# Optimization experiments

Hardware: AMD Instinct MI355X
Metric: run time of the kernel (lower is better)

The kernel has to match this reference:

```python
import jax, jax.numpy as jnp
import numpy as np

B, LQ, D, NH, NL, NP, DFFN = 16, 900, 256, 8, 4, 4, 2048
HD = D // NH
SHAPES = [(128, 128), (64, 64), (32, 32), (16, 16)]
LIN = sum(h * w for h, w in SHAPES)


def setup_inputs():
    ks = jax.random.split(jax.random.key(0), 24)
    p = lambda k, s: jax.random.normal(k, s, jnp.float32) * 0.02
    z = lambda s: jnp.zeros(s, jnp.float32)
    return {
        "queries": jax.random.normal(ks[0], (B, LQ, D), jnp.float32),
        "features": jax.random.normal(ks[1], (B, LIN, D), jnp.float32),
        "reference_points": jax.random.uniform(ks[2], (B, LQ, NL, 2), jnp.float32),
        "q_pos": jax.random.normal(ks[3], (B, LQ, D), jnp.float32),
        "in_proj_w": p(ks[4], (3 * D, D)), "in_proj_b": z((3 * D,)),
        "out_proj_w": p(ks[5], (D, D)), "out_proj_b": z((D,)),
        "value_proj_w": p(ks[6], (D, D)), "value_proj_b": z((D,)),
        "samp_w": p(ks[7], (NH * NL * NP * 2, D)),
        "samp_b": jax.random.uniform(ks[8], (NH * NL * NP * 2,), jnp.float32, -0.5, 0.5),
        "attw_w": p(ks[9], (NH * NL * NP, D)), "attw_b": z((NH * NL * NP,)),
        "msout_w": p(ks[10], (D, D)), "msout_b": z((D,)),
        "ffn_w1": p(ks[11], (DFFN, D)), "ffn_b1": z((DFFN,)),
        "ffn_w2": p(ks[12], (D, DFFN)), "ffn_b2": z((D,)),
        "ln1_g": jnp.ones((D,), jnp.float32), "ln1_b": z((D,)),
        "ln2_g": jnp.ones((D,), jnp.float32), "ln2_b": z((D,)),
        "ln3_g": jnp.ones((D,), jnp.float32), "ln3_b": z((D,)),
        "kv_spatial_shapes": np.array(SHAPES, np.int32),
        "level_start_index": np.concatenate([[0], np.cumsum([h * w for h, w in SHAPES])[:-1]]).astype(np.int32),
    }


def _ln(x, g, b, eps=1e-5):
    m = x.mean(-1, keepdims=True)
    v = ((x - m) ** 2).mean(-1, keepdims=True)
    return (x - m) * jax.lax.rsqrt(v + eps) * g + b


def _mha(q, k, v, wqkv, bqkv, wo, bo):
    wq, wk, wv = wqkv[:D], wqkv[D:2 * D], wqkv[2 * D:]
    bq, bk, bv = bqkv[:D], bqkv[D:2 * D], bqkv[2 * D:]
    qh = (q @ wq.T + bq).reshape(B, LQ, NH, HD)
    kh = (k @ wk.T + bk).reshape(B, LQ, NH, HD)
    vh = (v @ wv.T + bv).reshape(B, LQ, NH, HD)
    s = jnp.einsum("bqhd,bkhd->bhqk", qh, kh) / jnp.sqrt(jnp.float32(HD))
    a = jax.nn.softmax(s, axis=-1)
    o = jnp.einsum("bhqk,bkhd->bqhd", a, vh).reshape(B, LQ, D)
    return o @ wo.T + bo


def _ms_deform(value, loc, attw):
    # value (B,LIN,NH,HD); loc (B,LQ,NH,NL,NP,2) normalized; attw (B,LQ,NH,NL,NP)
    out = jnp.zeros((B, LQ, NH, HD), jnp.float32)
    start = 0
    for l, (hl, wl) in enumerate(SHAPES):
        v = value[:, start:start + hl * wl].transpose(0, 2, 1, 3)  # (B,NH,hl*wl,HD)
        g = loc[:, :, :, l]  # (B,LQ,NH,NP,2)
        # grid_sample align_corners=False pixel coords
        x = g[..., 0] * wl - 0.5
        y = g[..., 1] * hl - 0.5
        x0 = jnp.floor(x); y0 = jnp.floor(y)
        fx = x - x0; fy = y - y0
        x0 = x0.astype(jnp.int32); y0 = y0.astype(jnp.int32)
        acc = jnp.zeros((B, LQ, NH, NP, HD), jnp.float32)
        for dy, wy in ((0, 1.0 - fy), (1, fy)):
            for dx, wx in ((0, 1.0 - fx), (1, fx)):
                xi = x0 + dx; yi = y0 + dy
                valid = (xi >= 0) & (xi < wl) & (yi >= 0) & (yi < hl)
                idx = jnp.clip(yi, 0, hl - 1) * wl + jnp.clip(xi, 0, wl - 1)
                idx = idx.transpose(0, 2, 1, 3).reshape(B, NH, LQ * NP)
                s = jnp.take_along_axis(v, idx[..., None], axis=2)
                s = s.reshape(B, NH, LQ, NP, HD).transpose(0, 2, 1, 3, 4)
                w = jnp.where(valid, wy * wx, 0.0)  # zero-padding outside
                acc = acc + s * w[..., None]
        out = out + (acc * attw[:, :, :, l, :, None]).sum(3)
        start += hl * wl
    return out.reshape(B, LQ, D)


def reference(queries, features, reference_points, q_pos, in_proj_w, in_proj_b, out_proj_w, out_proj_b, value_proj_w, value_proj_b, samp_w, samp_b, attw_w, attw_b, msout_w, msout_b, ffn_w1, ffn_b1, ffn_w2, ffn_b2, ln1_g, ln1_b, ln2_g, ln2_b, ln3_g, ln3_b, kv_spatial_shapes, level_start_index):
    qk = queries + q_pos
    x = _ln(queries + _mha(qk, qk, queries, in_proj_w, in_proj_b, out_proj_w, out_proj_b), ln1_g, ln1_b)
    # deformable multi-scale cross attention
    q2 = x + q_pos
    value = (features @ value_proj_w.T + value_proj_b).reshape(B, LIN, NH, HD)
    off = (q2 @ samp_w.T + samp_b).reshape(B, LQ, NH, NL, NP, 2)
    attw = jax.nn.softmax((q2 @ attw_w.T + attw_b).reshape(B, LQ, NH, NL * NP), axis=-1).reshape(B, LQ, NH, NL, NP)
    norm = jnp.stack([jnp.asarray(kv_spatial_shapes)[:, 1], jnp.asarray(kv_spatial_shapes)[:, 0]], -1).astype(jnp.float32)  # (NL,2)=(W,H)
    loc = reference_points[:, :, None, :, None, :] + off / norm[None, None, None, :, None, :]
    ms = _ms_deform(value, loc, attw) @ msout_w.T + msout_b
    x = _ln(x + ms, ln2_g, ln2_b)
    ffn = jax.nn.relu(x @ ffn_w1.T + ffn_b1) @ ffn_w2.T + ffn_b2
    return _ln(x + ffn, ln3_g, ln3_b)
```

## Files before the change

kernel.cpp:

```cpp
#include <hip/hip_runtime.h>
#include <hip/hip_bf16.h>
#include <math.h>

#define B_    16
#define LQ_   900
#define D_    256
#define NH_   8
#define HD_   32
#define NL_   4
#define NP_   4
#define DFFN_ 2048
#define LIN_  21760

typedef unsigned short u16;
typedef __attribute__((ext_vector_type(8))) short bf16x8;
typedef __attribute__((ext_vector_type(4))) float f32x4;

__device__ __forceinline__ short f2bf(float f) {
    unsigned u = __float_as_uint(f);
    u += 0x7fffu + ((u >> 16) & 1u);
    return (short)(u >> 16);
}
__device__ __forceinline__ float bf2f(u16 u) {
    return __uint_as_float(((unsigned)u) << 16);
}

__global__ __launch_bounds__(256) void add_kernel(const float* __restrict__ a,
                                                  const float* __restrict__ b,
                                                  float* __restrict__ c,
                                                  size_t n4) {
    size_t i = (size_t)blockIdx.x * blockDim.x + threadIdx.x;
    if (i < n4) {
        float4 x = ((const float4*)a)[i];
        float4 y = ((const float4*)b)[i];
        ((float4*)c)[i] = make_float4(x.x + y.x, x.y + y.y, x.z + y.z, x.w + y.w);
    }
}

#define LDK 40
template <typename TA, typename TC>
__global__ __launch_bounds__(256) void gemm_t_kernel(const TA* __restrict__ A,
                                                     const float* __restrict__ W,
                                                     const float* __restrict__ bias,
                                                     const float* __restrict__ res,
                                                     TC* __restrict__ C,
                                                     int M, int N, int K, int relu) {
    __shared__ __align__(16) short As[128 * LDK];
    __shared__ __align__(16) short Bs[128 * LDK];

    const int n0 = blockIdx.x * 128;
    const int m0 = blockIdx.y * 128;
    const int t  = threadIdx.x;

    const int srow = t >> 1;
    const int scol = (t & 1) << 4;

    const int lane = t & 63;
    const int lr   = lane & 15;
    const int kg   = lane >> 4;
    const int wid  = t >> 6;
    const int wr   = wid >> 1;
    const int wc   = wid & 1;

    f32x4 acc[4][4] = {};

    const short* pA = &As[(wr * 64 + lr) * LDK + kg * 8];
    const short* pB = &Bs[(wc * 64 + lr) * LDK + kg * 8];

    for (int k0 = 0; k0 < K; k0 += 32) {
        {
            int gm = m0 + srow;
            if constexpr (sizeof(TA) == 4) {
                short tmp[16];
                if (gm < M) {
                    const float* src = (const float*)A + (size_t)gm * K + k0 + scol;
                    #pragma unroll
                    for (int q = 0; q < 4; ++q) {
                        float4 v = *(const float4*)(src + q * 4);
                        tmp[q * 4 + 0] = f2bf(v.x);
                        tmp[q * 4 + 1] = f2bf(v.y);
                        tmp[q * 4 + 2] = f2bf(v.z);
                        tmp[q * 4 + 3] = f2bf(v.w);
                    }
                } else {
                    #pragma unroll
                    for (int q = 0; q < 16; ++q) tmp[q] = 0;
                }
                *(bf16x8*)&As[srow * LDK + scol]     = *(bf16x8*)tmp;
                *(bf16x8*)&As[srow * LDK + scol + 8] = *(bf16x8*)(tmp + 8);
            } else {
                bf16x8 v0, v1;
                if (gm < M) {
                    const u16* src = (const u16*)A + (size_t)gm * K + k0 + scol;
                    v0 = *(const bf16x8*)src;
                    v1 = *(const bf16x8*)(src + 8);
                } else {
                    #pragma unroll
                    for (int q = 0; q < 8; ++q) { v0[q] = 0; v1[q] = 0; }
                }
                *(bf16x8*)&As[srow * LDK + scol]     = v0;
                *(bf16x8*)&As[srow * LDK + scol + 8] = v1;
            }
        }
        {
            short tmp[16];
            const float* src = W + (size_t)(n0 + srow) * K + k0 + scol;
            #pragma unroll
            for (int q = 0; q < 4; ++q) {
                float4 v = *(const float4*)(src + q * 4);
                tmp[q * 4 + 0] = f2bf(v.x);
                tmp[q * 4 + 1] = f2bf(v.y);
                tmp[q * 4 + 2] = f2bf(v.z);
                tmp[q * 4 + 3] = f2bf(v.w);
            }
            *(bf16x8*)&Bs[srow * LDK + scol]     = *(bf16x8*)tmp;
            *(bf16x8*)&Bs[srow * LDK + scol + 8] = *(bf16x8*)(tmp + 8);
        }
        __syncthreads();

        bf16x8 a[4], b[4];
        #pragma unroll
        for (int i = 0; i < 4; ++i) a[i] = *(const bf16x8*)(pA + i * 16 * LDK);
        #pragma unroll
        for (int j = 0; j < 4; ++j) b[j] = *(const bf16x8*)(pB + j * 16 * LDK);
        #pragma unroll
        for (int i = 0; i < 4; ++i)
            #pragma unroll
            for (int j = 0; j < 4; ++j)
                acc[i][j] = __builtin_amdgcn_mfma_f32_16x16x32_bf16(a[i], b[j], acc[i][j], 0, 0, 0);
        __syncthreads();
    }

    #pragma unroll
    for (int i = 0; i < 4; ++i) {
        #pragma unroll
        for (int j = 0; j < 4; ++j) {
            const int n = n0 + wc * 64 + j * 16 + lr;
            const float bn = bias[n];
            #pragma unroll
            for (int r = 0; r < 4; ++r) {
                const int m = m0 + wr * 64 + i * 16 + kg * 4 + r;
                if (m < M) {
                    float v = acc[i][j][r] + bn;
                    if (res)  v += res[(size_t)m * N + n];
                    if (relu) v = fmaxf(v, 0.f);
                    if constexpr (sizeof(TC) == 4) C[(size_t)m * N + n] = v;
                    else                           C[(size_t)m * N + n] = (TC)(u16)f2bf(v);
                }
            }
        }
    }
}

#define LDA2 40
#define LDP  72
__global__ __launch_bounds__(256) void attn_mfma_kernel(const u16* __restrict__ Qg,
                                                        const u16* __restrict__ Kg,
                                                        const u16* __restrict__ Vg,
                                                        u16* __restrict__ Og) {
    __shared__ __align__(16) u16 Ks[64 * LDA2];
    __shared__ __align__(16) u16 Vs[64 * LDA2];
    __shared__ __align__(16) u16 Ps[4][16 * LDP];

    const int qt = blockIdx.x, h = blockIdx.y, b = blockIdx.z;
    const int t  = threadIdx.x;
    const int wq = t >> 6;
    const int lane = t & 63;
    const int l15  = lane & 15;
    const int g    = lane >> 4;
    const int q0   = qt * 64;

    const int srow = t >> 2;
    const int sd   = (t & 3) * 8;

    int qrow = q0 + wq * 16 + l15;
    if (qrow > LQ_ - 1) qrow = LQ_ - 1;
    const bf16x8 qfrag = *(const bf16x8*)(Qg + ((size_t)(b * LQ_) + qrow) * D_ + h * HD_ + g * 8);

    float m_i = -1e30f, l_i = 0.f;
    f32x4 o_acc[2] = {};
    const float scale = 0.17677669529663687f;

    for (int k0 = 0; k0 < 960; k0 += 64) {
        {
            int kr = k0 + srow;
            bf16x8 kv, vv;
            if (kr < LQ_) {
                kv = *(const bf16x8*)(Kg + ((size_t)(b * LQ_) + kr) * D_ + h * HD_ + sd);
                vv = *(const bf16x8*)(Vg + ((size_t)(b * LQ_) + kr) * D_ + h * HD_ + sd);
            } else {
                #pragma unroll
                for (int j = 0; j < 8; ++j) { kv[j] = 0; vv[j] = 0; }
            }
            *(bf16x8*)&Ks[srow * LDA2 + sd] = kv;
            *(bf16x8*)&Vs[srow * LDA2 + sd] = vv;
        }
        __syncthreads();

        float p[4][4];
        float tmax = -1e30f;
        #pragma unroll
        for (int kt = 0; kt < 4; ++kt) {
            bf16x8 af = *(const bf16x8*)&Ks[(kt * 16 + l15) * LDA2 + g * 8];
            f32x4 c = {0.f, 0.f, 0.f, 0.f};
            c = __builtin_amdgcn_mfma_f32_16x16x32_bf16(af, qfrag, c, 0, 0, 0);
            #pragma unroll
            for (int r = 0; r < 4; ++r) {
                int kglob = k0 + kt * 16 + g * 4 + r;
                float s = (kglob < LQ_) ? c[r] * scale : -1e30f;
                p[kt][r] = s;
                tmax = fmaxf(tmax, s);
            }
        }
        tmax = fmaxf(tmax, __shfl_xor(tmax, 16));
        tmax = fmaxf(tmax, __shfl_xor(tmax, 32));
        float newm = fmaxf(m_i, tmax);
        float corr = __expf(m_i - newm);
        float rs = 0.f;
        #pragma unroll
        for (int kt = 0; kt < 4; ++kt) {
            #pragma unroll
            for (int r = 0; r < 4; ++r) {
                float e = __expf(p[kt][r] - newm);
                p[kt][r] = e;
                rs += e;
            }
            ushort4 pk;
            pk.x = (u16)f2bf(p[kt][0]);
            pk.y = (u16)f2bf(p[kt][1]);
            pk.z = (u16)f2bf(p[kt][2]);
            pk.w = (u16)f2bf(p[kt][3]);
            *(ushort4*)&Ps[wq][l15 * LDP + kt * 16 + g * 4] = pk;
        }
        rs += __shfl_xor(rs, 16);
        rs += __shfl_xor(rs, 32);
        l_i = l_i * corr + rs;
        m_i = newm;

        #pragma unroll
        for (int r = 0; r < 4; ++r) {
            float cq = __shfl(corr, g * 4 + r);
            o_acc[0][r] *= cq;
            o_acc[1][r] *= cq;
        }

        #pragma unroll
        for (int c = 0; c < 2; ++c) {
            bf16x8 pa = *(const bf16x8*)&Ps[wq][l15 * LDP + c * 32 + g * 8];
            #pragma unroll
            for (int nt = 0; nt < 2; ++nt) {
                short vv[8];
                #pragma unroll
                for (int j = 0; j < 8; ++j)
                    vv[j] = (short)Vs[(c * 32 + g * 8 + j) * LDA2 + nt * 16 + l15];
                o_acc[nt] = __builtin_amdgcn_mfma_f32_16x16x32_bf16(pa, *(bf16x8*)vv, o_acc[nt], 0, 0, 0);
            }
        }
        __syncthreads();
    }

    float il = 1.f / l_i;
    #pragma unroll
    for (int r = 0; r < 4; ++r) {
        float ilq = __shfl(il, g * 4 + r);
        int q = q0 + wq * 16 + g * 4 + r;
        if (q < LQ_) {
            u16* dst = Og + ((size_t)(b * LQ_) + q) * D_ + h * HD_ + l15;
            dst[0]  = (u16)f2bf(o_acc[0][r] * ilq);
            dst[16] = (u16)f2bf(o_acc[1][r] * ilq);
        }
    }
}

__global__ __launch_bounds__(256) void ln_kernel(const float* __restrict__ X,
                                                 const float* __restrict__ g,
                                                 const float* __restrict__ bb,
                                                 float* __restrict__ Y, int M) {
    int row  = blockIdx.x * 4 + (threadIdx.x >> 6);
    int lane = threadIdx.x & 63;
    if (row >= M) return;
    const float* x = X + (size_t)row * D_;
    float4 v = *(const float4*)(x + lane * 4);
    float s = v.x + v.y + v.z + v.w;
    #pragma unroll
    for (int o = 32; o >= 1; o >>= 1) s += __shfl_xor(s, o);
    float mean = s * (1.f / D_);
    float dx0 = v.x - mean, dx1 = v.y - mean, dx2 = v.z - mean, dx3 = v.w - mean;
    float ss = dx0 * dx0 + dx1 * dx1 + dx2 * dx2 + dx3 * dx3;
    #pragma unroll
    for (int o = 32; o >= 1; o >>= 1) ss += __shfl_xor(ss, o);
    float rstd = rsqrtf(ss * (1.f / D_) + 1e-5f);
    float4 gv = *(const float4*)(g + lane * 4);
    float4 bv = *(const float4*)(bb + lane * 4);
    float4 out;
    out.x = dx0 * rstd * gv.x + bv.x;
    out.y = dx1 * rstd * gv.y + bv.y;
    out.z = dx2 * rstd * gv.z + bv.z;
    out.w = dx3 * rstd * gv.w + bv.w;
    *(float4*)(Y + (size_t)row * D_ + lane * 4) = out;
}

__global__ __launch_bounds__(256) void softmax16_kernel(const float* __restrict__ X,
                                                        float* __restrict__ Y,
                                                        int rows) {
    int r = blockIdx.x * blockDim.x + threadIdx.x;
    if (r >= rows) return;
    const float* x = X + (size_t)r * 16;
    float m = -1e30f;
    #pragma unroll
    for (int i = 0; i < 16; ++i) m = fmaxf(m, x[i]);
    float e[16], s = 0.f;
    #pragma unroll
    for (int i = 0; i < 16; ++i) { e[i] = expf(x[i] - m); s += e[i]; }
    float inv = 1.f / s;
    float* y = Y + (size_t)r * 16;
    #pragma unroll
    for (int i = 0; i < 16; ++i) y[i] = e[i] * inv;
}

__global__ __launch_bounds__(256) void msdeform_kernel(const u16* __restrict__ value,
                                                       const float* __restrict__ ref,
                                                       const float* __restrict__ off,
                                                       const float* __restrict__ attw,
                                                       float* __restrict__ out) {
    const int levH[4] = {128, 64, 32, 16};
    const int levW[4] = {128, 64, 32, 16};
    const int levS[4] = {0, 16384, 20480, 21504};

    int gid = blockIdx.x * 256 + threadIdx.x;
    int d   = gid & (HD_ - 1);
    int bqh = gid >> 5;
    int h   = bqh & (NH_ - 1);
    int bq  = bqh >> 3;
    int b   = bq / LQ_;

    const float* refp = ref + (size_t)bq * NL_ * 2;
    const float* offp = off + (size_t)bq * (NH_ * NL_ * NP_ * 2) + h * (NL_ * NP_ * 2);
    const float* awp  = attw + (size_t)bq * (NH_ * NL_ * NP_) + h * (NL_ * NP_);
    const u16* vbase  = value + (size_t)b * LIN_ * D_ + h * HD_ + d;

    float o = 0.f;
    #pragma unroll
    for (int l = 0; l < NL_; ++l) {
        float rx = refp[l * 2 + 0], ry = refp[l * 2 + 1];
        int wl = levW[l], hl = levH[l];
        const u16* vlev = vbase + (size_t)levS[l] * D_;
        #pragma unroll
        for (int p = 0; p < NP_; ++p) {
            float ox = offp[(l * NP_ + p) * 2 + 0];
            float oy = offp[(l * NP_ + p) * 2 + 1];
            float x = rx * wl + ox - 0.5f;
            float y = ry * hl + oy - 0.5f;
            float x0f = floorf(x), y0f = floorf(y);
            float fx = x - x0f, fy = y - y0f;
            int x0 = (int)x0f, y0 = (int)y0f;
            float aw = awp[l * NP_ + p];
            float sacc = 0.f;
            #pragma unroll
            for (int dy = 0; dy < 2; ++dy) {
                int  yi = y0 + dy;
                float wy = dy ? fy : 1.f - fy;
                bool vy = (yi >= 0) && (yi < hl);
                int  yc = min(max(yi, 0), hl - 1);
                #pragma unroll
                for (int dx = 0; dx < 2; ++dx) {
                    int  xi = x0 + dx;
                    float wx = dx ? fx : 1.f - fx;
                    bool vx = (xi >= 0) && (xi < wl);
                    int  xc = min(max(xi, 0), wl - 1);
                    float w  = (vx && vy) ? wy * wx : 0.f;
                    float sv = bf2f(vlev[(size_t)(yc * wl + xc) * D_]);
                    sacc += w * sv;
                }
            }
            o += aw * sacc;
        }
    }
    out[gid] = o;
}

extern "C" void kernel_launch(void* const* d_in, const int* in_sizes, int n_in,
                              void* d_out, int out_size, void* d_ws, size_t ws_size,
                              hipStream_t stream) {
    const float* queries      = (const float*)d_in[0];
    const float* features     = (const float*)d_in[1];
    const float* refpts       = (const float*)d_in[2];
    const float* q_pos        = (const float*)d_in[3];
    const float* in_proj_w    = (const float*)d_in[4];
    const float* in_proj_b    = (const float*)d_in[5];
    const float* out_proj_w   = (const float*)d_in[6];
    const float* out_proj_b   = (const float*)d_in[7];
    const float* value_proj_w = (const float*)d_in[8];
    const float* value_proj_b = (const float*)d_in[9];
    const float* samp_w       = (const float*)d_in[10];
    const float* samp_b       = (const float*)d_in[11];
    const float* attw_w       = (const float*)d_in[12];
    const float* attw_b       = (const float*)d_in[13];
    const float* msout_w      = (const float*)d_in[14];
    const float* msout_b      = (const float*)d_in[15];
    const float* ffn_w1       = (const float*)d_in[16];
    const float* ffn_b1       = (const float*)d_in[17];
    const float* ffn_w2       = (const float*)d_in[18];
    const float* ffn_b2       = (const float*)d_in[19];
    const float* ln1_g        = (const float*)d_in[20];
    const float* ln1_b        = (const float*)d_in[21];
    const float* ln2_g        = (const float*)d_in[22];
    const float* ln2_b        = (const float*)d_in[23];
    const float* ln3_g        = (const float*)d_in[24];
    const float* ln3_b        = (const float*)d_in[25];

    float* ws = (float*)d_ws;
    const size_t NQ = (size_t)B_ * LQ_ * D_;
    float* bufA = ws;
    float* bufB = ws + NQ;
    float* bufC = ws + 2 * NQ;
    float* bufD = ws + 3 * NQ;
    float* bufF = ws + 4 * NQ;
    u16* VALb = (u16*)(ws + 5 * NQ);
    u16* H1b  = VALb + (size_t)B_ * LIN_ * D_;
    u16* Qb   = H1b + (size_t)B_ * LQ_ * DFFN_;
    u16* Kb   = Qb + NQ;
    u16* Vb   = Kb + NQ;
    u16* Ob   = Vb + NQ;

    const int M  = B_ * LQ_;
    const int MV = B_ * LIN_;
    const int GY = (M + 127) / 128;

    add_kernel<<<3600, 256, 0, stream>>>(queries, q_pos, bufA, NQ / 4);

    gemm_t_kernel<float, u16><<<dim3(2, GY), 256, 0, stream>>>(bufA, in_proj_w,          in_proj_b,       nullptr, Qb, M, 256, 256, 0);
    gemm_t_kernel<float, u16><<<dim3(2, GY), 256, 0, stream>>>(bufA, in_proj_w + 65536,  in_proj_b + 256, nullptr, Kb, M, 256, 256, 0);
    gemm_t_kernel<float, u16><<<dim3(2, GY), 256, 0, stream>>>(queries, in_proj_w + 131072, in_proj_b + 512, nullptr, Vb, M, 256, 256, 0);

    attn_mfma_kernel<<<dim3(15, NH_, B_), 256, 0, stream>>>(Qb, Kb, Vb, Ob);

    gemm_t_kernel<u16, float><<<dim3(2, GY), 256, 0, stream>>>(Ob, out_proj_w, out_proj_b, queries, bufB, M, 256, 256, 0);
    ln_kernel<<<3600, 256, 0, stream>>>(bufB, ln1_g, ln1_b, bufF, M);

    add_kernel<<<3600, 256, 0, stream>>>(bufF, q_pos, bufA, NQ / 4);

    gemm_t_kernel<float, u16><<<dim3(2, MV / 128), 256, 0, stream>>>(features, value_proj_w, value_proj_b, nullptr, VALb, MV, 256, 256, 0);

    gemm_t_kernel<float, float><<<dim3(2, GY), 256, 0, stream>>>(bufA, samp_w, samp_b, nullptr, bufB, M, 256, 256, 0);
    gemm_t_kernel<float, float><<<dim3(1, GY), 256, 0, stream>>>(bufA, attw_w, attw_b, nullptr, bufC, M, 128, 256, 0);

    softmax16_kernel<<<450, 256, 0, stream>>>(bufC, bufD, B_ * LQ_ * NH_);

    msdeform_kernel<<<14400, 256, 0, stream>>>(VALb, refpts, bufB, bufD, bufA);

    gemm_t_kernel<float, float><<<dim3(2, GY), 256, 0, stream>>>(bufA, msout_w, msout_b, bufF, bufB, M, 256, 256, 0);
    ln_kernel<<<3600, 256, 0, stream>>>(bufB, ln2_g, ln2_b, bufC, M);

    gemm_t_kernel<float, u16><<<dim3(16, GY), 256, 0, stream>>>(bufC, ffn_w1, ffn_b1, nullptr, H1b, M, 2048, 256, 1);

    gemm_t_kernel<u16, float><<<dim3(2, GY), 256, 0, stream>>>(H1b, ffn_w2, ffn_b2, bufC, bufA, M, 256, 2048, 0);
    ln_kernel<<<3600, 256, 0, stream>>>(bufA, ln3_g, ln3_b, (float*)d_out, M);
}
```

Baseline: 1.196 ms.

## Pre-convert weights to bf16, double-buffer GEMM, vectorize deformable sampling

Adds a kernel that converts all weight matrices to bf16 once per call, so GEMMs no longer convert weights to bf16 on every tile load. Intermediate activations (qk sums, LN2 output, msdeform output) are now emitted in bf16 to halve operand traffic. The GEMM is rewritten with double-buffered LDS and register prefetch, dropping one barrier per k-step. The deformable sampling kernel now has each thread handle 8 channels with 128-bit loads. The extra bf16 rounding of activations may change numerics slightly.

```diff
diff --git a/kernel.cpp b/kernel.cpp
--- a/kernel.cpp
+++ b/kernel.cpp
@@ -25,28 +25,75 @@
     return __uint_as_float(((unsigned)u) << 16);
 }
 
-__global__ __launch_bounds__(256) void add_kernel(const float* __restrict__ a,
-                                                  const float* __restrict__ b,
-                                                  float* __restrict__ c,
-                                                  size_t n4) {
+#define WOFF_INPROJ  0
+#define WOFF_OUTPROJ 196608
+#define WOFF_VALPROJ 262144
+#define WOFF_SAMP    327680
+#define WOFF_ATTW    393216
+#define WOFF_MSOUT   425984
+#define WOFF_FFN1    491520
+#define WOFF_FFN2    1015808
+#define WTOTAL       1540096
+
+__global__ __launch_bounds__(256) void wprep_kernel(const float* __restrict__ s0,
+                                                    const float* __restrict__ s1,
+                                                    const float* __restrict__ s2,
+                                                    const float* __restrict__ s3,
+                                                    const float* __restrict__ s4,
+                                                    const float* __restrict__ s5,
+                                                    const float* __restrict__ s6,
+                                                    const float* __restrict__ s7,
+                                                    u16* __restrict__ Wb) {
+    int i8 = (blockIdx.x * 256 + threadIdx.x) * 8;
+    if (i8 >= WTOTAL) return;
+    const float* src; int rel;
+    if      (i8 < WOFF_OUTPROJ) { src = s0; rel = i8; }
+    else if (i8 < WOFF_VALPROJ) { src = s1; rel = i8 - WOFF_OUTPROJ; }
+    else if (i8 < WOFF_SAMP)    { src = s2; rel = i8 - WOFF_VALPROJ; }
+    else if (i8 < WOFF_ATTW)    { src = s3; rel = i8 - WOFF_SAMP; }
+    else if (i8 < WOFF_MSOUT)   { src = s4; rel = i8 - WOFF_ATTW; }
+    else if (i8 < WOFF_FFN1)    { src = s5; rel = i8 - WOFF_MSOUT; }
+    else if (i8 < WOFF_FFN2)    { src = s6; rel = i8 - WOFF_FFN1; }
+    else                        { src = s7; rel = i8 - WOFF_FFN2; }
+    float4 v0 = *(const float4*)(src + rel);
+    float4 v1 = *(const float4*)(src + rel + 4);
+    short o[8];
+    o[0] = f2bf(v0.x); o[1] = f2bf(v0.y); o[2] = f2bf(v0.z); o[3] = f2bf(v0.w);
+    o[4] = f2bf(v1.x); o[5] = f2bf(v1.y); o[6] = f2bf(v1.z); o[7] = f2bf(v1.w);
+    *(bf16x8*)(Wb + i8) = *(bf16x8*)o;
+}
+
+__global__ __launch_bounds__(256) void add_bf16_kernel(const float* __restrict__ a,
+                                                       const float* __restrict__ b,
+                                                       u16* __restrict__ osum,
+                                                       u16* __restrict__ oa,
+                                                       size_t n4) {
     size_t i = (size_t)blockIdx.x * blockDim.x + threadIdx.x;
-    if (i < n4) {
-        float4 x = ((const float4*)a)[i];
-        float4 y = ((const float4*)b)[i];
-        ((float4*)c)[i] = make_float4(x.x + y.x, x.y + y.y, x.z + y.z, x.w + y.w);
+    if (i >= n4) return;
+    float4 x = ((const float4*)a)[i];
+    float4 y = ((const float4*)b)[i];
+    ushort4 s;
+    s.x = (u16)f2bf(x.x + y.x); s.y = (u16)f2bf(x.y + y.y);
+    s.z = (u16)f2bf(x.z + y.z); s.w = (u16)f2bf(x.w + y.w);
+    ((ushort4*)osum)[i] = s;
+    if (oa) {
+        ushort4 q;
+        q.x = (u16)f2bf(x.x); q.y = (u16)f2bf(x.y);
+        q.z = (u16)f2bf(x.z); q.w = (u16)f2bf(x.w);
+        ((ushort4*)oa)[i] = q;
     }
 }
 
 #define LDK 40
 template <typename TA, typename TC>
-__global__ __launch_bounds__(256) void gemm_t_kernel(const TA* __restrict__ A,
-                                                     const float* __restrict__ W,
-                                                     const float* __restrict__ bias,
-                                                     const float* __restrict__ res,
-                                                     TC* __restrict__ C,
-                                                     int M, int N, int K, int relu) {
-    __shared__ __align__(16) short As[128 * LDK];
-    __shared__ __align__(16) short Bs[128 * LDK];
+__global__ __launch_bounds__(256) void gemm2_kernel(const TA* __restrict__ A,
+                                                    const u16* __restrict__ W,
+                                                    const float* __restrict__ bias,
+                                                    const float* __restrict__ res,
+                                                    TC* __restrict__ C,
+                                                    int M, int N, int K, int relu) {
+    __shared__ __align__(16) u16 As[2][128 * LDK];
+    __shared__ __align__(16) u16 Bs[2][128 * LDK];
 
     const int n0 = blockIdx.x * 128;
     const int m0 = blockIdx.y * 128;
@@ -64,60 +111,77 @@
 
     f32x4 acc[4][4] = {};
 
-    const short* pA = &As[(wr * 64 + lr) * LDK + kg * 8];
-    const short* pB = &Bs[(wc * 64 + lr) * LDK + kg * 8];
-
-    for (int k0 = 0; k0 < K; k0 += 32) {
-        {
-            int gm = m0 + srow;
+    const int  nk  = K >> 5;
+    const int  gm  = m0 + srow;
+    const bool mok = (gm < M);
+
+    const float* af32 = (const float*)A + (size_t)(mok ? gm : 0) * K + scol;
+    const u16*   ab16 = (const u16*)A + (size_t)(mok ? gm : 0) * K + scol;
+    const u16*   wp   = W + (size_t)(n0 + srow) * K + scol;
+
+    float4 af[4];
+    bf16x8 ab[2];
+    bf16x8 wf[2];
+
+    if constexpr (sizeof(TA) == 4) {
+        if (mok) {
+            #pragma unroll
+            for (int q = 0; q < 4; ++q) af[q] = *(const float4*)(af32 + q * 4);
+        } else {
+            #pragma unroll
+            for (int q = 0; q < 4; ++q) af[q] = make_float4(0.f, 0.f, 0.f, 0.f);
+        }
+    } else {
+        if (mok) { ab[0] = *(const bf16x8*)ab16; ab[1] = *(const bf16x8*)(ab16 + 8); }
+        else {
+            #pragma unroll
+            for (int q = 0; q < 8; ++q) { ab[0][q] = 0; ab[1][q] = 0; }
+        }
+    }
+    wf[0] = *(const bf16x8*)wp;
+    wf[1] = *(const bf16x8*)(wp + 8);
+
+    for (int kt = 0; kt < nk; ++kt) {
+        const int cur = kt & 1;
+        if constexpr (sizeof(TA) == 4) {
+            short tmp[16];
+            #pragma unroll
+            for (int q = 0; q < 4; ++q) {
+                tmp[q * 4 + 0] = f2bf(af[q].x);
+                tmp[q * 4 + 1] = f2bf(af[q].y);
+                tmp[q * 4 + 2] = f2bf(af[q].z);
+                tmp[q * 4 + 3] = f2bf(af[q].w);
+            }
+            *(bf16x8*)&As[cur][srow * LDK + scol]     = *(bf16x8*)tmp;
+            *(bf16x8*)&As[cur][srow * LDK + scol + 8] = *(bf16x8*)(tmp + 8);
+        } else {
+            *(bf16x8*)&As[cur][srow * LDK + scol]     = ab[0];
+            *(bf16x8*)&As[cur][srow * LDK + scol + 8] = ab[1];
+        }
+        *(bf16x8*)&Bs[cur][srow * LDK + scol]     = wf[0];
+        *(bf16x8*)&Bs[cur][srow * LDK + scol + 8] = wf[1];
+
+        if (kt + 1 < nk) {
+            const int k1 = (kt + 1) << 5;
             if constexpr (sizeof(TA) == 4) {
-                short tmp[16];
-                if (gm < M) {
-                    const float* src = (const float*)A + (size_t)gm * K + k0 + scol;
+                if (mok) {
                     #pragma unroll
-                    for (int q = 0; q < 4; ++q) {
-                        float4 v = *(const float4*)(src + q * 4);
-                        tmp[q * 4 + 0] = f2bf(v.x);
-                        tmp[q * 4 + 1] = f2bf(v.y);
-                        tmp[q * 4 + 2] = f2bf(v.z);
-                        tmp[q * 4 + 3] = f2bf(v.w);
-                    }
-                } else {
-                    #pragma unroll
-                    for (int q = 0; q < 16; ++q) tmp[q] = 0;
+                    for (int q = 0; q < 4; ++q) af[q] = *(const float4*)(af32 + k1 + q * 4);
                 }
-                *(bf16x8*)&As[srow * LDK + scol]     = *(bf16x8*)tmp;
-                *(bf16x8*)&As[srow * LDK + scol + 8] = *(bf16x8*)(tmp + 8);
             } else {
-                bf16x8 v0, v1;
-                if (gm < M) {
-                    const u16* src = (const u16*)A + (size_t)gm * K + k0 + scol;
-                    v0 = *(const bf16x8*)src;
-                    v1 = *(const bf16x8*)(src + 8);
-                } else {
-                    #pragma unroll
-                    for (int q = 0; q < 8; ++q) { v0[q] = 0; v1[q] = 0; }
+                if (mok) {
+                    ab[0] = *(const bf16x8*)(ab16 + k1);
+                    ab[1] = *(const bf16x8*)(ab16 + k1 + 8);
                 }
-                *(bf16x8*)&As[srow * LDK + scol]     = v0;
-                *(bf16x8*)&As[srow * LDK + scol + 8] = v1;
-            }
-        }
-        {
-            short tmp[16];
-            const float* src = W + (size_t)(n0 + srow) * K + k0 + scol;
-            #pragma unroll
-            for (int q = 0; q < 4; ++q) {
-                float4 v = *(const float4*)(src + q * 4);
-                tmp[q * 4 + 0] = f2bf(v.x);
-                tmp[q * 4 + 1] = f2bf(v.y);
-                tmp[q * 4 + 2] = f2bf(v.z);
-                tmp[q * 4 + 3] = f2bf(v.w);
-            }
-            *(bf16x8*)&Bs[srow * LDK + scol]     = *(bf16x8*)tmp;
-            *(bf16x8*)&Bs[srow * LDK + scol + 8] = *(bf16x8*)(tmp + 8);
-        }
+            }
+            wf[0] = *(const bf16x8*)(wp + k1);
+            wf[1] = *(const bf16x8*)(wp + k1 + 8);
+        }
+
         __syncthreads();
 
+        const u16* pA = &As[cur][(wr * 64 + lr) * LDK + kg * 8];
+        const u16* pB = &Bs[cur][(wc * 64 + lr) * LDK + kg * 8];
         bf16x8 a[4], b[4];
         #pragma unroll
         for (int i = 0; i < 4; ++i) a[i] = *(const bf16x8*)(pA + i * 16 * LDK);
@@ -128,7 +192,6 @@
             #pragma unroll
             for (int j = 0; j < 4; ++j)
                 acc[i][j] = __builtin_amdgcn_mfma_f32_16x16x32_bf16(a[i], b[j], acc[i][j], 0, 0, 0);
-        __syncthreads();
     }
 
     #pragma unroll
@@ -275,7 +338,8 @@
 __global__ __launch_bounds__(256) void ln_kernel(const float* __restrict__ X,
                                                  const float* __restrict__ g,
                                                  const float* __restrict__ bb,
-                                                 float* __restrict__ Y, int M) {
+                                                 float* __restrict__ Y,
+                                                 u16* __restrict__ Yb, int M) {
     int row  = blockIdx.x * 4 + (threadIdx.x >> 6);
     int lane = threadIdx.x & 63;
     if (row >= M) return;
@@ -298,6 +362,12 @@
     out.z = dx2 * rstd * gv.z + bv.z;
     out.w = dx3 * rstd * gv.w + bv.w;
     *(float4*)(Y + (size_t)row * D_ + lane * 4) = out;
+    if (Yb) {
+        ushort4 ob;
+        ob.x = (u16)f2bf(out.x); ob.y = (u16)f2bf(out.y);
+        ob.z = (u16)f2bf(out.z); ob.w = (u16)f2bf(out.w);
+        *(ushort4*)(Yb + (size_t)row * D_ + lane * 4) = ob;
+    }
 }
 
 __global__ __launch_bounds__(256) void softmax16_kernel(const float* __restrict__ X,
@@ -318,32 +388,32 @@
     for (int i = 0; i < 16; ++i) y[i] = e[i] * inv;
 }
 
-__global__ __launch_bounds__(256) void msdeform_kernel(const u16* __restrict__ value,
-                                                       const float* __restrict__ ref,
-                                                       const float* __restrict__ off,
-                                                       const float* __restrict__ attw,
-                                                       float* __restrict__ out) {
+__global__ __launch_bounds__(256) void msdeform2_kernel(const u16* __restrict__ value,
+                                                        const float* __restrict__ ref,
+                                                        const float* __restrict__ off,
+                                                        const float* __restrict__ attw,
+                                                        u16* __restrict__ out) {
     const int levH[4] = {128, 64, 32, 16};
     const int levW[4] = {128, 64, 32, 16};
     const int levS[4] = {0, 16384, 20480, 21504};
 
     int gid = blockIdx.x * 256 + threadIdx.x;
-    int d   = gid & (HD_ - 1);
-    int bqh = gid >> 5;
+    int d8  = gid & 3;
+    int bqh = gid >> 2;
     int h   = bqh & (NH_ - 1);
     int bq  = bqh >> 3;
     int b   = bq / LQ_;
 
-    const float* refp = ref + (size_t)bq * NL_ * 2;
-    const float* offp = off + (size_t)bq * (NH_ * NL_ * NP_ * 2) + h * (NL_ * NP_ * 2);
-    const float* awp  = attw + (size_t)bq * (NH_ * NL_ * NP_) + h * (NL_ * NP_);
-    const u16* vbase  = value + (size_t)b * LIN_ * D_ + h * HD_ + d;
-
-    float o = 0.f;
+    const float* refp = ref  + (size_t)bq * NL_ * 2;
+    const float* offp = off  + (size_t)bq * 256 + h * 32;
+    const float* awp  = attw + (size_t)bq * 128 + h * 16;
+    const u16* vbase  = value + (size_t)b * LIN_ * D_ + h * HD_ + d8 * 8;
+
+    float acc[8] = {};
     #pragma unroll
     for (int l = 0; l < NL_; ++l) {
         float rx = refp[l * 2 + 0], ry = refp[l * 2 + 1];
-        int wl = levW[l], hl = levH[l];
+        const int wl = levW[l], hl = levH[l];
         const u16* vlev = vbase + (size_t)levS[l] * D_;
         #pragma unroll
         for (int p = 0; p < NP_; ++p) {
@@ -355,28 +425,31 @@
             float fx = x - x0f, fy = y - y0f;
             int x0 = (int)x0f, y0 = (int)y0f;
             float aw = awp[l * NP_ + p];
-            float sacc = 0.f;
             #pragma unroll
             for (int dy = 0; dy < 2; ++dy) {
-                int  yi = y0 + dy;
+                int   yi = y0 + dy;
                 float wy = dy ? fy : 1.f - fy;
-                bool vy = (yi >= 0) && (yi < hl);
-                int  yc = min(max(yi, 0), hl - 1);
+                bool  vy = (yi >= 0) && (yi < hl);
+                int   yc = min(max(yi, 0), hl - 1);
                 #pragma unroll
                 for (int dx = 0; dx < 2; ++dx) {
-                    int  xi = x0 + dx;
+                    int   xi = x0 + dx;
                     float wx = dx ? fx : 1.f - fx;
-                    bool vx = (xi >= 0) && (xi < wl);
-                    int  xc = min(max(xi, 0), wl - 1);
-                    float w  = (vx && vy) ? wy * wx : 0.f;
-                    float sv = bf2f(vlev[(size_t)(yc * wl + xc) * D_]);
-                    sacc += w * sv;
+                    bool  vx = (xi >= 0) && (xi < wl);
+                    int   xc = min(max(xi, 0), wl - 1);
+                    float w  = (vx && vy) ? aw * wy * wx : 0.f;
+                    bf16x8 v = *(const bf16x8*)(vlev + (size_t)(yc * wl + xc) * D_);
+                    #pragma unroll
+                    for (int j = 0; j < 8; ++j)
+                        acc[j] += w * bf2f((u16)v[j]);
                 }
             }
-            o += aw * sacc;
-        }
-    }
-    out[gid] = o;
+        }
+    }
+    short o[8];
+    #pragma unroll
+    for (int j = 0; j < 8; ++j) o[j] = f2bf(acc[j]);
+    *(bf16x8*)(out + (size_t)bq * D_ + h * HD_ + d8 * 8) = *(bf16x8*)o;
 }
 
 extern "C" void kernel_launch(void* const* d_in, const int* in_sizes, int n_in,
@@ -411,49 +484,58 @@
 
     float* ws = (float*)d_ws;
     const size_t NQ = (size_t)B_ * LQ_ * D_;
-    float* bufA = ws;
-    float* bufB = ws + NQ;
-    float* bufC = ws + 2 * NQ;
+    float* bufB = ws;
+    float* bufC = ws + NQ;
+    float* bufF = ws + 2 * NQ;
     float* bufD = ws + 3 * NQ;
-    float* bufF = ws + 4 * NQ;
-    u16* VALb = (u16*)(ws + 5 * NQ);
+    u16* U    = (u16*)(ws + 4 * NQ);
+    u16* qkb  = U;
+    u16* qb   = U + NQ;
+    u16* q2b  = U + 2 * NQ;
+    u16* Qb   = U + 3 * NQ;
+    u16* Kb   = U + 4 * NQ;
+    u16* Vb   = U + 5 * NQ;
+    u16* Ob   = U + 6 * NQ;
+    u16* MSb  = U + 7 * NQ;
+    u16* LN2b = U + 8 * NQ;
+    u16* VALb = U + 9 * NQ;
     u16* H1b  = VALb + (size_t)B_ * LIN_ * D_;
-    u16* Qb   = H1b + (size_t)B_ * LQ_ * DFFN_;
-    u16* Kb   = Qb + NQ;
-    u16* Vb   = Kb + NQ;
-    u16* Ob   = Vb + NQ;
+    u16* Wb   = H1b + (size_t)B_ * LQ_ * DFFN_;
 
     const int M  = B_ * LQ_;
     const int MV = B_ * LIN_;
     const int GY = (M + 127) / 128;
 
-    add_kernel<<<3600, 256, 0, stream>>>(queries, q_pos, bufA, NQ / 4);
-
-    gemm_t_kernel<float, u16><<<dim3(2, GY), 256, 0, stream>>>(bufA, in_proj_w,          in_proj_b,       nullptr, Qb, M, 256, 256, 0);
-    gemm_t_kernel<float, u16><<<dim3(2, GY), 256, 0, stream>>>(bufA, in_proj_w + 65536,  in_proj_b + 256, nullptr, Kb, M, 256, 256, 0);
-    gemm_t_kernel<float, u16><<<dim3(2, GY), 256, 0, stream>>>(queries, in_proj_w + 131072, in_proj_b + 512, nullptr, Vb, M, 256, 256, 0);
+    wprep_kernel<<<752, 256, 0, stream>>>(in_proj_w, out_proj_w, value_proj_w, samp_w,
+                                          attw_w, msout_w, ffn_w1, ffn_w2, Wb);
+
+    add_bf16_kernel<<<3600, 256, 0, stream>>>(queries, q_pos, qkb, qb, NQ / 4);
+
+    gemm2_kernel<u16, u16><<<dim3(2, GY), 256, 0, stream>>>(qkb, Wb + WOFF_INPROJ,          in_proj_b,       nullptr, Qb, M, 256, 256, 0);
+    gemm2_kernel<u16, u16><<<dim3(2, GY), 256, 0, stream>>>(qkb, Wb + WOFF_INPROJ + 65536,  in_proj_b + 256, nullptr, Kb, M, 256, 256, 0);
+    gemm2_kernel<u16, u16><<<dim3(2, GY), 256, 0, stream>>>(qb,  Wb + WOFF_INPROJ + 131072, in_proj_b + 512, nullptr, Vb, M, 256, 256, 0);
 
     attn_mfma_kernel<<<dim3(15, NH_, B_), 256, 0, stream>>>(Qb, Kb, Vb, Ob);
 
-    gemm_t_kernel<u16, float><<<dim3(2, GY), 256, 0, stream>>>(Ob, out_proj_w, out_proj_b, queries, bufB, M, 256, 256, 0);
-    ln_kernel<<<3600, 256, 0, stream>>>(bufB, ln1_g, ln1_b, bufF, M);
-
-    add_kernel<<<3600, 256, 0, stream>>>(bufF, q_pos, bufA, NQ / 4);
-
-    gemm_t_kernel<float, u16><<<dim3(2, MV / 128), 256, 0, stream>>>(features, value_proj_w, value_proj_b, nullptr, VALb, MV, 256, 256, 0);
-
-    gemm_t_kernel<float, float><<<dim3(2, GY), 256, 0, stream>>>(bufA, samp_w, samp_b, nullptr, bufB, M, 256, 256, 0);
-    gemm_t_kernel<float, float><<<dim3(1, GY), 256, 0, stream>>>(bufA, attw_w, attw_b, nullptr, bufC, M, 128, 256, 0);
+    gemm2_kernel<u16, float><<<dim3(2, GY), 256, 0, stream>>>(Ob, Wb + WOFF_OUTPROJ, out_proj_b, queries, bufB, M, 256, 256, 0);
+    ln_kernel<<<3600, 256, 0, stream>>>(bufB, ln1_g, ln1_b, bufF, nullptr, M);
+
+    add_bf16_kernel<<<3600, 256, 0, stream>>>(bufF, q_pos, q2b, nullptr, NQ / 4);
+
+    gemm2_kernel<float, u16><<<dim3(2, MV / 128), 256, 0, stream>>>(features, Wb + WOFF_VALPROJ, value_proj_b, nullptr, VALb, MV, 256, 256, 0);
+
+    gemm2_kernel<u16, float><<<dim3(2, GY), 256, 0, stream>>>(q2b, Wb + WOFF_SAMP, samp_b, nullptr, bufB, M, 256, 256, 0);
+    gemm2_kernel<u16, float><<<dim3(1, GY), 256, 0, stream>>>(q2b, Wb + WOFF_ATTW, attw_b, nullptr, bufC, M, 128, 256, 0);
 
     softmax16_kernel<<<450, 256, 0, stream>>>(bufC, bufD, B_ * LQ_ * NH_);
 
-    msdeform_kernel<<<14400, 256, 0, stream>>>(VALb, refpts, bufB, bufD, bufA);
-
-    gemm_t_kernel<float, float><<<dim3(2, GY), 256, 0, stream>>>(bufA, msout_w, msout_b, bufF, bufB, M, 256, 256, 0);
-    ln_kernel<<<3600, 256, 0, stream>>>(bufB, ln2_g, ln2_b, bufC, M);
-
-    gemm_t_kernel<float, u16><<<dim3(16, GY), 256, 0, stream>>>(bufC, ffn_w1, ffn_b1, nullptr, H1b, M, 2048, 256, 1);
-
-    gemm_t_kernel<u16, float><<<dim3(2, GY), 256, 0, stream>>>(H1b, ffn_w2, ffn_b2, bufC, bufA, M, 256, 2048, 0);
-    ln_kernel<<<3600, 256, 0, stream>>>(bufA, ln3_g, ln3_b, (float*)d_out, M);
-}
+    msdeform2_kernel<<<1800, 256, 0, stream>>>(VALb, refpts, bufB, bufD, MSb);
+
+    gemm2_kernel<u16, float><<<dim3(2, GY), 256, 0, stream>>>(MSb, Wb + WOFF_MSOUT, msout_b, bufF, bufB, M, 256, 256, 0);
+    ln_kernel<<<3600, 256, 0, stream>>>(bufB, ln2_g, ln2_b, bufC, LN2b, M);
+
+    gemm2_kernel<u16, u16><<<dim3(16, GY), 256, 0, stream>>>(LN2b, Wb + WOFF_FFN1, ffn_b1, nullptr, H1b, M, 2048, 256, 1);
+
+    gemm2_kernel<u16, float><<<dim3(2, GY), 256, 0, stream>>>(H1b, Wb + WOFF_FFN2, ffn_b2, bufC, bufB, M, 256, 2048, 0);
+    ln_kernel<<<3600, 256, 0, stream>>>(bufB, ln3_g, ln3_b, (float*)d_out, nullptr, M);
+}
```

Result: faster. 1.055 ms (-11.7%).
